# Performance work log

Measured on AMD Instinct MI355X. Metric: run time of the kernel, lower is better.

The kernel has to match this reference:

```python
import jax, jax.numpy as jnp
import numpy as np

V, E, H0, H1 = 32000, 512, 1024, 1024
B, S = 32, 128


def setup_inputs() -> dict:
    key = jax.random.key(0)
    ks = jax.random.split(key, 10)
    s = 0.02
    tokens = jax.random.randint(ks[0], (B, S), 0, V)
    emb = jax.random.normal(ks[1], (V, E), dtype=jnp.float32) * s
    W0 = jax.random.normal(ks[2], (E, H0), dtype=jnp.float32) * s
    U0 = jax.random.normal(ks[3], (H0, H0), dtype=jnp.float32) * s
    b0 = jnp.zeros((H0,), dtype=jnp.float32)
    W1 = jax.random.normal(ks[4], (H0, H1), dtype=jnp.float32) * s
    U1 = jax.random.normal(ks[5], (H1, H1), dtype=jnp.float32) * s
    b1 = jnp.zeros((H1,), dtype=jnp.float32)
    Wd = jax.random.normal(ks[6], (H1, V), dtype=jnp.float32) * s
    bd = jnp.zeros((V,), dtype=jnp.float32)
    return {"tokens": tokens, "emb": emb, "W0": W0, "U0": U0, "b0": b0,
            "W1": W1, "U1": U1, "b1": b1, "Wd": Wd, "bd": bd}


def reference(tokens, emb, W0, U0, b0, W1, U1, b1, Wd, bd):
    # Embedding lookup: [B, S, E]
    x = emb[tokens]
    # Stacked SimpleRNN: h_t = tanh(x W + h U + b), layer1 feeds layer2 per step.
    xt = jnp.swapaxes(x, 0, 1)  # [S, B, E] for scan over time

    def step(carry, x_t):
        h0, h1 = carry
        h0 = jnp.tanh(x_t @ W0 + h0 @ U0 + b0)
        h1 = jnp.tanh(h0 @ W1 + h1 @ U1 + b1)
        return (h0, h1), h1

    batch = tokens.shape[0]
    init = (jnp.zeros((batch, W0.shape[1]), dtype=x.dtype),
            jnp.zeros((batch, W1.shape[1]), dtype=x.dtype))
    _, ys = jax.lax.scan(step, init, xt)  # ys: [S, B, H1]
    ys = jnp.swapaxes(ys, 0, 1)  # [B, S, H1]
    # Final dense to vocab logits: [B, S, V]
    return ys @ Wd + bd
```

## Files before the change

### kernel.cpp

```cpp
#include <hip/hip_runtime.h>
#include <hip/hip_bf16.h>
#include <cstdint>

typedef __attribute__((ext_vector_type(8))) short bf16x8;
typedef __attribute__((ext_vector_type(4))) float f32x4;
typedef __attribute__((ext_vector_type(4))) unsigned int u32x4;

#define V_ 32000
#define E_ 512
#define H_ 1024
#define B_ 32
#define S_ 128

#define L1WG 16
#define L2WG 32
#define NWGS 48
#define NTILES 250
#define GWGS (16 * NTILES)

typedef __attribute__((address_space(1))) unsigned int* gas1_t;
typedef __attribute__((address_space(3))) unsigned int* las3_t;
__device__ __forceinline__ void load_lds16(const void* g, void* l) {
  __builtin_amdgcn_global_load_lds((gas1_t)g, (las3_t)l, 16, 0, 0);
}

__device__ __forceinline__ void ldx4_sc(u32x4* d, const void* p) {
  asm volatile("global_load_dwordx4 %0, %1, off sc0 sc1" : "=v"(*d) : "v"(p) : "memory");
}
__device__ __forceinline__ unsigned ld_sc(const unsigned* p) {
  unsigned d;
  asm volatile("global_load_dword %0, %1, off sc0 sc1\n\ts_waitcnt vmcnt(0)"
               : "=v"(d) : "v"(p) : "memory");
  return d;
}
__device__ __forceinline__ void st_swap(unsigned* p, unsigned v) {
  asm volatile("global_atomic_swap %0, %1, off sc1" :: "v"(p), "v"(v) : "memory");
}
__device__ __forceinline__ void st_swap2(uint2* p, uint2 v) {
  asm volatile("global_atomic_swap_x2 %0, %1, off sc1" :: "v"(p), "v"(v) : "memory");
}
#define WAITVM0()                                     \
  asm volatile("s_waitcnt vmcnt(0)" ::: "memory");    \
  __builtin_amdgcn_sched_barrier(0)

__device__ __forceinline__ unsigned short bfbits(float x) {
  __hip_bfloat16 b = __float2bfloat16(x);
  union { __hip_bfloat16 b; unsigned short u; } c;
  c.b = b;
  return c.u;
}

__device__ __forceinline__ uint2 pack_rows(const float f[4], int lane, int j) {
  uint2 v2[4];
#pragma unroll
  for (int r = 0; r < 4; ++r) {
    const float o = __shfl_xor(f[r], 1);
    const float lo = (lane & 1) ? o : f[r];
    const float hi = (lane & 1) ? f[r] : o;
    const unsigned pk = (unsigned)bfbits(lo) | ((unsigned)bfbits(hi) << 16);
    const unsigned q2 = __shfl_xor(pk, 2);
    v2[r].x = (j & 2) ? q2 : pk;
    v2[r].y = (j & 2) ? pk : q2;
  }
  const int rs = lane & 3;
  return rs == 0 ? v2[0] : rs == 1 ? v2[1] : rs == 2 ? v2[2] : v2[3];
}

__global__ __launch_bounds__(256) void transpose_f32_bf16(
    const float* __restrict__ src, __hip_bfloat16* __restrict__ dst, int R, int C) {
  __shared__ float tile[32][33];
  const int c0 = blockIdx.x << 5, r0 = blockIdx.y << 5;
  const int tx = threadIdx.x & 31, ty = threadIdx.x >> 5;
#pragma unroll
  for (int i = 0; i < 32; i += 8)
    tile[ty + i][tx] = src[(size_t)(r0 + ty + i) * C + (c0 + tx)];
  __syncthreads();
#pragma unroll
  for (int i = 0; i < 32; i += 8)
    dst[(size_t)(c0 + ty + i) * R + (r0 + tx)] = __float2bfloat16(tile[tx][ty + i]);
}

__global__ __launch_bounds__(256) void gather_embed(
    const int* __restrict__ tokens, const float* __restrict__ emb,
    __hip_bfloat16* __restrict__ Xg) {
  const int r = blockIdx.x;
  const int t = r >> 5, b = r & 31;
  const int tok = tokens[b * S_ + t];
  const float* e = emb + (size_t)tok * E_;
  __hip_bfloat16* o = Xg + (size_t)r * E_;
  for (int k = threadIdx.x; k < E_; k += 256) o[k] = __float2bfloat16(e[k]);
}

__global__ __launch_bounds__(256) void make_frag_w(
    const float* __restrict__ W, __hip_bfloat16* __restrict__ F, int ncols) {
  const int idx = blockIdx.x * 256 + threadIdx.x;
  const int lane = idx & 63, kb = (idx >> 6) & 31, g = idx >> 11;
  const int j = (g << 4) + (lane & 15);
  const int kbase = (kb << 5) + ((lane >> 4) << 3);
  __hip_bfloat16* o = F + (size_t)idx * 8;
#pragma unroll
  for (int e = 0; e < 8; ++e) o[e] = __float2bfloat16(W[(size_t)(kbase + e) * ncols + j]);
}

__global__ __launch_bounds__(256) void gemm_bf16_tn(
    const __hip_bfloat16* __restrict__ A, const __hip_bfloat16* __restrict__ Bt,
    const float* __restrict__ bias, float* __restrict__ C, int M, int N, int K) {
  __shared__ __hip_bfloat16 ldsA[2][128 * 64];
  __shared__ __hip_bfloat16 ldsB[2][128 * 64];
  const int nwg = gridDim.x * gridDim.y;
  int L = blockIdx.y * gridDim.x + blockIdx.x;
  L = ((L & 7) * (nwg >> 3)) + (L >> 3);
  const int m0 = (L / gridDim.x) << 7;
  const int n0 = (L % gridDim.x) << 7;
  const int tid = threadIdx.x, wave = tid >> 6, lane = tid & 63;
  const int wr = wave >> 1, wc = wave & 1;
  f32x4 acc[4][4];
#pragma unroll
  for (int i = 0; i < 4; ++i)
#pragma unroll
    for (int jj = 0; jj < 4; ++jj) acc[i][jj] = (f32x4){0.f, 0.f, 0.f, 0.f};

  auto stage = [&](int buf, int k0) {
#pragma unroll
    for (int i = 0; i < 4; ++i) {
      const int c = i * 4 + wave;
      const int idx = (c << 6) + lane;
      const int row = idx >> 3, kk = (idx & 7) << 3;
      load_lds16(A + (size_t)(m0 + row) * K + (k0 + kk), &ldsA[buf][c * 512]);
      load_lds16(Bt + (size_t)(n0 + row) * K + (k0 + kk), &ldsB[buf][c * 512]);
    }
  };
  stage(0, 0);
  __syncthreads();
  int cur = 0;
  for (int k0 = 0; k0 < K; k0 += 64) {
    if (k0 + 64 < K) stage(cur ^ 1, k0 + 64);
    __builtin_amdgcn_s_setprio(1);
#pragma unroll
    for (int ks = 0; ks < 2; ++ks) {
      bf16x8 af[4], bfr[4];
#pragma unroll
      for (int mi = 0; mi < 4; ++mi)
        af[mi] = *(const bf16x8*)(&ldsA[cur][0] +
                                  (((wr << 6) + (mi << 4) + (lane & 15)) << 6) +
                                  (ks << 5) + ((lane >> 4) << 3));
#pragma unroll
      for (int ni = 0; ni < 4; ++ni)
        bfr[ni] = *(const bf16x8*)(&ldsB[cur][0] +
                                   (((wc << 6) + (ni << 4) + (lane & 15)) << 6) +
                                   (ks << 5) + ((lane >> 4) << 3));
#pragma unroll
      for (int mi = 0; mi < 4; ++mi)
#pragma unroll
        for (int ni = 0; ni < 4; ++ni)
          acc[mi][ni] =
              __builtin_amdgcn_mfma_f32_16x16x32_bf16(af[mi], bfr[ni], acc[mi][ni], 0, 0, 0);
    }
    __builtin_amdgcn_s_setprio(0);
    __syncthreads();
    cur ^= 1;
  }
#pragma unroll
  for (int mi = 0; mi < 4; ++mi) {
#pragma unroll
    for (int ni = 0; ni < 4; ++ni) {
      const int n = n0 + (wc << 6) + (ni << 4) + (lane & 15);
      const float bn = bias[n];
#pragma unroll
      for (int r = 0; r < 4; ++r) {
        const int m = m0 + (wr << 6) + (mi << 4) + ((lane >> 4) << 2) + r;
        C[(size_t)m * N + n] = acc[mi][ni][r] + bn;
      }
    }
  }
}

__global__ __launch_bounds__(512, 1) void rnn_vocab_fused(
    const __hip_bfloat16* __restrict__ U0f, const __hip_bfloat16* __restrict__ W1f,
    const __hip_bfloat16* __restrict__ U1f, const float* __restrict__ xw,
    const float* __restrict__ b1,
    __hip_bfloat16* __restrict__ h0buf,
    __hip_bfloat16* __restrict__ h1buf,
    __hip_bfloat16* __restrict__ Yf,
    unsigned* __restrict__ flags,
    const __hip_bfloat16* __restrict__ Wdf,
    const float* __restrict__ bd, float* __restrict__ out) {
  __shared__ char smem[135168];
  const int tid = threadIdx.x, wave = tid >> 6, lane = tid & 63;

  if (blockIdx.x < NWGS) {
    char* sA0 = smem;
    char* sA1 = smem + 65536;
    float* pad = (float*)(smem + 131072);
    const int g = blockIdx.x;
    const bool isL1 = (g < L1WG);
    const int mi = wave & 1;
    const int cg = isL1 ? (wave >> 1) : ((wave >> 1) & 1);
    const int mat = isL1 ? 0 : (wave >> 2);
    const int colbase = isL1 ? (g << 6) : ((g - L1WG) << 5);
    const int j = colbase + (cg << 4) + (lane & 15);
    const int gg = (colbase >> 4) + cg;
    const int rowbase = (mi << 4) + ((lane >> 4) << 2);
    const int rs = lane & 3;
    const int ra = (mi << 4) + (lane & 15);
    const int q4 = (lane >> 4) << 4;
    const float b1j = b1[j];

    const __hip_bfloat16* wb = isL1 ? U0f : (mat == 0 ? W1f : U1f);
    bf16x8 wfr[32];
#pragma unroll
    for (int kb = 0; kb < 32; ++kb)
      wfr[kb] = *(const bf16x8*)(wb + (size_t)((((gg << 5) + kb) << 6) + lane) * 8);

    if (!isL1) {
      for (int i = tid; i < 4096; i += 512) *(uint4*)(sA1 + i * 16) = (uint4){0u, 0u, 0u, 0u};
    }
    __syncthreads();

    const int stg_row = tid >> 7;
    const int stg_colb = (tid & 127) << 4;
    const unsigned* fpoll = flags + ((lane < NWGS ? lane : NWGS - 1) << 4);

    if (isL1) {
      for (int p = 0; p < S_; ++p) {
        const float* xrow = xw + ((size_t)p << 15);
        float xv[4];
#pragma unroll
        for (int r = 0; r < 4; ++r) xv[r] = xrow[(rowbase + r) * H_ + j];
        if (p >= 1) {
          const unsigned tgt =
              (lane < L1WG) ? (unsigned)p : (p >= 3 ? (unsigned)(p - 3) : 0u);
          unsigned v;
          do { v = ld_sc(fpoll); } while (__any(v < tgt));
          const char* src0 = (const char*)(h0buf + ((size_t)((p - 1) & 3) << 15));
          u32x4 t0[8];
#pragma unroll
          for (int i = 0; i < 8; ++i) ldx4_sc(&t0[i], src0 + (size_t)(((i << 9) + tid) << 4));
          WAITVM0();
#pragma unroll
          for (int i = 0; i < 8; ++i) {
            const int row = stg_row + (i << 2);
            *(u32x4*)(sA0 + (row << 11) + (stg_colb ^ ((row & 7) << 4))) = t0[i];
          }
          __syncthreads();
        }
        f32x4 acc = {0.f, 0.f, 0.f, 0.f};
        if (p >= 1) {
#pragma unroll
          for (int kb = 0; kb < 32; ++kb) {
            bf16x8 a = *(const bf16x8*)(
                sA0 + (ra << 11) + ((((kb << 6) + q4)) ^ ((ra & 7) << 4)));
            acc = __builtin_amdgcn_mfma_f32_16x16x32_bf16(a, wfr[kb], acc, 0, 0, 0);
          }
        }
        float f[4];
#pragma unroll
        for (int r = 0; r < 4; ++r) f[r] = tanhf(acc[r] + xv[r]);
        uint2 vsel = pack_rows(f, lane, j);
        uint2* h4 = (uint2*)(h0buf + ((size_t)(p & 3) << 15));
        st_swap2(h4 + (rowbase + rs) * (H_ / 4) + (j >> 2), vsel);
        WAITVM0();
        __syncthreads();
        if (tid == 0) st_swap(flags + (g << 4), (unsigned)(p + 1));
      }
    } else {
      for (int t = 0; t < S_; ++t) {
        {
          const unsigned tgt = (lane < L1WG) ? (unsigned)(t + 1) : (unsigned)t;
          unsigned v;
          do { v = ld_sc(fpoll); } while (__any(v < tgt));
        }
        {
          const char* src0 = (const char*)(h0buf + ((size_t)(t & 3) << 15));
          u32x4 t0[8], t1[8];
#pragma unroll
          for (int i = 0; i < 8; ++i) ldx4_sc(&t0[i], src0 + (size_t)(((i << 9) + tid) << 4));
          if (t >= 1) {
            const char* src1 = (const char*)(h1buf + ((size_t)((t - 1) & 1) << 15));
#pragma unroll
            for (int i = 0; i < 8; ++i) ldx4_sc(&t1[i], src1 + (size_t)(((i << 9) + tid) << 4));
          }
          WAITVM0();
#pragma unroll
          for (int i = 0; i < 8; ++i) {
            const int row = stg_row + (i << 2);
            *(u32x4*)(sA0 + (row << 11) + (stg_colb ^ ((row & 7) << 4))) = t0[i];
          }
          if (t >= 1) {
#pragma unroll
            for (int i = 0; i < 8; ++i) {
              const int row = stg_row + (i << 2);
              *(u32x4*)(sA1 + (row << 11) + (stg_colb ^ ((row & 7) << 4))) = t1[i];
            }
          }
          __syncthreads();
        }
        const char* sA = (mat == 0) ? sA0 : sA1;
        f32x4 acc = {0.f, 0.f, 0.f, 0.f};
#pragma unroll
        for (int kb = 0; kb < 32; ++kb) {
          bf16x8 a = *(const bf16x8*)(
              sA + (ra << 11) + ((((kb << 6) + q4)) ^ ((ra & 7) << 4)));
          acc = __builtin_amdgcn_mfma_f32_16x16x32_bf16(a, wfr[kb], acc, 0, 0, 0);
        }
        const int pair = wave & 3;
        if (mat == 0) *(f32x4*)(pad + pair * 256 + lane * 4) = acc;
        __syncthreads();
        if (mat == 1) {
          f32x4 accW = *(const f32x4*)(pad + pair * 256 + lane * 4);
          float f[4];
#pragma unroll
          for (int r = 0; r < 4; ++r) f[r] = tanhf(acc[r] + accW[r] + b1j);
          uint2 vsel = pack_rows(f, lane, j);
          const int bb = rowbase + rs;
          uint2* h4 = (uint2*)(h1buf + ((size_t)(t & 1) << 15));
          st_swap2(h4 + bb * (H_ / 4) + (j >> 2), vsel);
          const int jb = j & ~3;
          const size_t fo =
              (((size_t)((t << 1) + (bb >> 4)) << 5) + (jb >> 5)) * 64 +
              (((jb >> 3) & 3) << 4) + (bb & 15);
          st_swap2((uint2*)((char*)Yf + fo * 16 + ((jb & 7) << 1)), vsel);
        }
        WAITVM0();
        __syncthreads();
        if (tid == 0) st_swap(flags + (g << 4), (unsigned)(t + 1));
      }
    }
    return;
  }

  const int bid = blockIdx.x - NWGS;
  const int mt = bid / NTILES, nt = bid - mt * NTILES;
  const int m0 = mt << 8, n0 = nt << 7;
  {
    const unsigned tgt = (unsigned)((mt << 3) + 8);
    if (wave == 0) {
      const unsigned* fp = flags + ((L1WG + (lane & 31)) << 4);
      while (true) {
        unsigned v = ld_sc(fp);
        if (!__any(v < tgt)) break;
        asm volatile("s_sleep 8");
      }
    }
    __syncthreads();
  }
  const int wr = wave >> 1, wc = wave & 1;
  f32x4 acc[4][4];
#pragma unroll
  for (int i = 0; i < 4; ++i)
#pragma unroll
    for (int jj = 0; jj < 4; ++jj) acc[i][jj] = (f32x4){0.f, 0.f, 0.f, 0.f};

  const char* Yc = (const char*)Yf;
  const char* Wc = (const char*)Wdf;
  auto stageA = [&](int buf, int k0) {
#pragma unroll
    for (int i = 0; i < 4; ++i) {
      const int c = (i << 3) + wave;
      const int mg = c >> 1, kb = c & 1;
      const char* src = Yc + ((((size_t)(m0 >> 4) + mg) << 5) + (k0 >> 5) + kb) * 1024 +
                        (lane << 4);
      load_lds16(src, smem + buf * 32768 + c * 1024);
    }
  };
  auto stageB = [&](int buf, int k0) {
#pragma unroll
    for (int i = 0; i < 2; ++i) {
      const int c = (i << 3) + wave;
      const int ng = c >> 1, kb = c & 1;
      const char* src = Wc + ((((size_t)(n0 >> 4) + ng) << 5) + (k0 >> 5) + kb) * 1024 +
                        (lane << 4);
      load_lds16(src, smem + 65536 + buf * 16384 + c * 1024);
    }
  };

  stageA(0, 0);
  stageB(0, 0);
  __syncthreads();
  int cur = 0;
  for (int k0 = 0; k0 < H_; k0 += 64) {
    if (k0 + 64 < H_) {
      stageA(cur ^ 1, k0 + 64);
      stageB(cur ^ 1, k0 + 64);
    }
    __builtin_amdgcn_s_setprio(1);
#pragma unroll
    for (int ks = 0; ks < 2; ++ks) {
      bf16x8 af[4], bfr[4];
#pragma unroll
      for (int mi = 0; mi < 4; ++mi)
        af[mi] = *(const bf16x8*)(smem + cur * 32768 +
                                  ((((wr << 2) + mi) << 1) + ks) * 1024 + (lane << 4));
#pragma unroll
      for (int ni = 0; ni < 4; ++ni)
        bfr[ni] = *(const bf16x8*)(smem + 65536 + cur * 16384 +
                                   ((((wc << 2) + ni) << 1) + ks) * 1024 + (lane << 4));
#pragma unroll
      for (int mi = 0; mi < 4; ++mi)
#pragma unroll
        for (int ni = 0; ni < 4; ++ni)
          acc[mi][ni] =
              __builtin_amdgcn_mfma_f32_16x16x32_bf16(af[mi], bfr[ni], acc[mi][ni], 0, 0, 0);
    }
    __builtin_amdgcn_s_setprio(0);
    __syncthreads();
    cur ^= 1;
  }
#pragma unroll
  for (int mi = 0; mi < 4; ++mi) {
#pragma unroll
    for (int ni = 0; ni < 4; ++ni) {
      const int n = n0 + (wc << 6) + (ni << 4) + (lane & 15);
      const float bn = bd[n];
#pragma unroll
      for (int r = 0; r < 4; ++r) {
        const int m = m0 + (wr << 6) + (mi << 4) + ((lane >> 4) << 2) + r;
        const size_t orow = (size_t)(m & 31) * S_ + (m >> 5);
        out[orow * V_ + n] = acc[mi][ni][r] + bn;
      }
    }
  }
}

extern "C" void kernel_launch(void* const* d_in, const int* in_sizes, int n_in, void* d_out,
                              int out_size, void* d_ws, size_t ws_size, hipStream_t stream) {
  const int* tokens = (const int*)d_in[0];
  const float* emb = (const float*)d_in[1];
  const float* W0 = (const float*)d_in[2];
  const float* U0 = (const float*)d_in[3];
  const float* b0 = (const float*)d_in[4];
  const float* W1 = (const float*)d_in[5];
  const float* U1 = (const float*)d_in[6];
  const float* b1 = (const float*)d_in[7];
  const float* Wd = (const float*)d_in[8];
  const float* bd = (const float*)d_in[9];
  float* out = (float*)d_out;

  char* ws = (char*)d_ws;
  __hip_bfloat16* Wdf = (__hip_bfloat16*)ws;  ws += (size_t)V_ * H_ * 2;
  __hip_bfloat16* W0t = (__hip_bfloat16*)ws;  ws += (size_t)H_ * E_ * 2;
  __hip_bfloat16* Xg = (__hip_bfloat16*)ws;   ws += (size_t)4096 * E_ * 2;
  __hip_bfloat16* U0f = (__hip_bfloat16*)ws;  ws += (size_t)H_ * H_ * 2;
  __hip_bfloat16* W1f = (__hip_bfloat16*)ws;  ws += (size_t)H_ * H_ * 2;
  __hip_bfloat16* U1f = (__hip_bfloat16*)ws;  ws += (size_t)H_ * H_ * 2;
  float* xw = (float*)ws;                     ws += (size_t)4096 * H_ * 4;
  __hip_bfloat16* h0buf = (__hip_bfloat16*)ws; ws += 4 * B_ * H_ * 2;
  __hip_bfloat16* h1buf = (__hip_bfloat16*)ws; ws += 2 * B_ * H_ * 2;
  __hip_bfloat16* Yf = (__hip_bfloat16*)ws;   ws += (size_t)4096 * H_ * 2;
  unsigned* flags = (unsigned*)ws;            ws += 4096;

  transpose_f32_bf16<<<dim3(H_ / 32, E_ / 32), 256, 0, stream>>>(W0, W0t, E_, H_);
  gather_embed<<<4096, 256, 0, stream>>>(tokens, emb, Xg);
  make_frag_w<<<512, 256, 0, stream>>>(U0, U0f, H_);
  make_frag_w<<<512, 256, 0, stream>>>(W1, W1f, H_);
  make_frag_w<<<512, 256, 0, stream>>>(U1, U1f, H_);
  make_frag_w<<<16000, 256, 0, stream>>>(Wd, Wdf, V_);
  hipMemsetAsync(flags, 0, 4096, stream);

  gemm_bf16_tn<<<dim3(H_ / 128, 4096 / 128), 256, 0, stream>>>(Xg, W0t, b0, xw, 4096, H_, E_);

  rnn_vocab_fused<<<NWGS + GWGS, 512, 0, stream>>>(U0f, W1f, U1f, xw, b1, h0buf, h1buf, Yf,
                                                   flags, Wdf, bd, out);
}
```

Before: 1.084 ms.

## Make output GEMM persistent over N-tiles with deeper prefetch pipeline

Replaces the 4000 one-tile GEMM workgroups with 208 persistent workgroups. Each one loops over its N-tiles and all 16 M-tiles in order, waiting on the RNN progress flags before each M-tile. The K loop now prefetches two stages ahead, using explicit vmcnt(6) waits and split barriers in place of a full wait each iteration. This is meant to cut launch and scheduling overhead, keep the Wd tile hot across M-tiles, and overlap loads with MFMA. The risk is load imbalance, since 250 tiles over 208 workgroups leaves some with two tiles, and the ordering is stricter against RNN completion.

```diff
diff --git a/kernel.cpp b/kernel.cpp
--- a/kernel.cpp
+++ b/kernel.cpp
@@ -16,7 +16,7 @@
 #define L2WG 32
 #define NWGS 48
 #define NTILES 250
-#define GWGS (16 * NTILES)
+#define GWGS 208
 
 typedef __attribute__((address_space(1))) unsigned int* gas1_t;
 typedef __attribute__((address_space(3))) unsigned int* las3_t;
@@ -41,6 +41,9 @@
 }
 #define WAITVM0()                                     \
   asm volatile("s_waitcnt vmcnt(0)" ::: "memory");    \
+  __builtin_amdgcn_sched_barrier(0)
+#define WAITVM6()                                     \
+  asm volatile("s_waitcnt vmcnt(6)" ::: "memory");    \
   __builtin_amdgcn_sched_barrier(0)
 
 __device__ __forceinline__ unsigned short bfbits(float x) {
@@ -329,94 +332,111 @@
     return;
   }
 
-  const int bid = blockIdx.x - NWGS;
-  const int mt = bid / NTILES, nt = bid - mt * NTILES;
-  const int m0 = mt << 8, n0 = nt << 7;
-  {
-    const unsigned tgt = (unsigned)((mt << 3) + 8);
-    if (wave == 0) {
-      const unsigned* fp = flags + ((L1WG + (lane & 31)) << 4);
-      while (true) {
-        unsigned v = ld_sc(fp);
-        if (!__any(v < tgt)) break;
-        asm volatile("s_sleep 8");
-      }
-    }
-    __syncthreads();
-  }
+  const int wg = blockIdx.x - NWGS;
   const int wr = wave >> 1, wc = wave & 1;
-  f32x4 acc[4][4];
-#pragma unroll
-  for (int i = 0; i < 4; ++i)
-#pragma unroll
-    for (int jj = 0; jj < 4; ++jj) acc[i][jj] = (f32x4){0.f, 0.f, 0.f, 0.f};
-
   const char* Yc = (const char*)Yf;
   const char* Wc = (const char*)Wdf;
-  auto stageA = [&](int buf, int k0) {
-#pragma unroll
-    for (int i = 0; i < 4; ++i) {
-      const int c = (i << 3) + wave;
-      const int mg = c >> 1, kb = c & 1;
-      const char* src = Yc + ((((size_t)(m0 >> 4) + mg) << 5) + (k0 >> 5) + kb) * 1024 +
-                        (lane << 4);
-      load_lds16(src, smem + buf * 32768 + c * 1024);
-    }
-  };
-  auto stageB = [&](int buf, int k0) {
-#pragma unroll
-    for (int i = 0; i < 2; ++i) {
-      const int c = (i << 3) + wave;
-      const int ng = c >> 1, kb = c & 1;
-      const char* src = Wc + ((((size_t)(n0 >> 4) + ng) << 5) + (k0 >> 5) + kb) * 1024 +
-                        (lane << 4);
-      load_lds16(src, smem + 65536 + buf * 16384 + c * 1024);
-    }
-  };
-
-  stageA(0, 0);
-  stageB(0, 0);
-  __syncthreads();
-  int cur = 0;
-  for (int k0 = 0; k0 < H_; k0 += 64) {
-    if (k0 + 64 < H_) {
-      stageA(cur ^ 1, k0 + 64);
-      stageB(cur ^ 1, k0 + 64);
-    }
-    __builtin_amdgcn_s_setprio(1);
-#pragma unroll
-    for (int ks = 0; ks < 2; ++ks) {
-      bf16x8 af[4], bfr[4];
-#pragma unroll
-      for (int mi = 0; mi < 4; ++mi)
-        af[mi] = *(const bf16x8*)(smem + cur * 32768 +
-                                  ((((wr << 2) + mi) << 1) + ks) * 1024 + (lane << 4));
-#pragma unroll
-      for (int ni = 0; ni < 4; ++ni)
-        bfr[ni] = *(const bf16x8*)(smem + 65536 + cur * 16384 +
-                                   ((((wc << 2) + ni) << 1) + ks) * 1024 + (lane << 4));
-#pragma unroll
-      for (int mi = 0; mi < 4; ++mi)
-#pragma unroll
-        for (int ni = 0; ni < 4; ++ni)
-          acc[mi][ni] =
-              __builtin_amdgcn_mfma_f32_16x16x32_bf16(af[mi], bfr[ni], acc[mi][ni], 0, 0, 0);
-    }
-    __builtin_amdgcn_s_setprio(0);
-    __syncthreads();
-    cur ^= 1;
-  }
-#pragma unroll
-  for (int mi = 0; mi < 4; ++mi) {
-#pragma unroll
-    for (int ni = 0; ni < 4; ++ni) {
-      const int n = n0 + (wc << 6) + (ni << 4) + (lane & 15);
-      const float bn = bd[n];
-#pragma unroll
-      for (int r = 0; r < 4; ++r) {
-        const int m = m0 + (wr << 6) + (mi << 4) + ((lane >> 4) << 2) + r;
-        const size_t orow = (size_t)(m & 31) * S_ + (m >> 5);
-        out[orow * V_ + n] = acc[mi][ni][r] + bn;
+
+  for (int nt = wg; nt < NTILES; nt += GWGS) {
+    const int n0 = nt << 7;
+    for (int mt = 0; mt < 16; ++mt) {
+      const int m0 = mt << 8;
+      {
+        const unsigned tgt = (unsigned)((mt << 3) + 8);
+        if (wave == 0) {
+          const unsigned* fp = flags + ((L1WG + (lane & 31)) << 4);
+          while (true) {
+            unsigned v = ld_sc(fp);
+            if (!__any(v < tgt)) break;
+            asm volatile("s_sleep 4");
+          }
+        }
+        __syncthreads();
+      }
+      f32x4 acc[4][4];
+#pragma unroll
+      for (int i = 0; i < 4; ++i)
+#pragma unroll
+        for (int jj = 0; jj < 4; ++jj) acc[i][jj] = (f32x4){0.f, 0.f, 0.f, 0.f};
+
+      auto stageA = [&](int buf, int k0) {
+#pragma unroll
+        for (int i = 0; i < 4; ++i) {
+          const int c = (i << 3) + wave;
+          const char* src = Yc +
+              ((((size_t)(m0 >> 4) + (c >> 1)) << 5) + (k0 >> 5) + (c & 1)) * 1024 +
+              (lane << 4);
+          load_lds16(src, smem + buf * 32768 + c * 1024);
+        }
+      };
+      auto stageB = [&](int buf, int k0) {
+#pragma unroll
+        for (int i = 0; i < 2; ++i) {
+          const int c = (i << 3) + wave;
+          const char* src = Wc +
+              ((((size_t)(n0 >> 4) + (c >> 1)) << 5) + (k0 >> 5) + (c & 1)) * 1024 +
+              (lane << 4);
+          load_lds16(src, smem + 65536 + buf * 16384 + c * 1024);
+        }
+      };
+
+      stageA(0, 0);
+      stageB(0, 0);
+      stageA(1, 64);
+      stageB(1, 64);
+      WAITVM6();
+      __builtin_amdgcn_sched_barrier(0);
+      __builtin_amdgcn_s_barrier();
+      int cur = 0;
+      for (int k0 = 0; k0 < H_; k0 += 64) {
+        __builtin_amdgcn_s_setprio(1);
+#pragma unroll
+        for (int ks = 0; ks < 2; ++ks) {
+          bf16x8 af[4], bfr[4];
+#pragma unroll
+          for (int mi = 0; mi < 4; ++mi)
+            af[mi] = *(const bf16x8*)(smem + cur * 32768 +
+                                      ((((wr << 2) + mi) << 1) + ks) * 1024 + (lane << 4));
+#pragma unroll
+          for (int ni = 0; ni < 4; ++ni)
+            bfr[ni] = *(const bf16x8*)(smem + 65536 + cur * 16384 +
+                                       ((((wc << 2) + ni) << 1) + ks) * 1024 + (lane << 4));
+#pragma unroll
+          for (int mi = 0; mi < 4; ++mi)
+#pragma unroll
+            for (int ni = 0; ni < 4; ++ni)
+              acc[mi][ni] = __builtin_amdgcn_mfma_f32_16x16x32_bf16(af[mi], bfr[ni],
+                                                                    acc[mi][ni], 0, 0, 0);
+        }
+        __builtin_amdgcn_s_setprio(0);
+        if (k0 + 64 < H_) {
+          __builtin_amdgcn_sched_barrier(0);
+          __builtin_amdgcn_s_barrier();
+          if (k0 + 128 < H_) {
+            stageA(cur, k0 + 128);
+            stageB(cur, k0 + 128);
+            WAITVM6();
+          } else {
+            WAITVM0();
+          }
+          __builtin_amdgcn_sched_barrier(0);
+          __builtin_amdgcn_s_barrier();
+          cur ^= 1;
+        }
+      }
+#pragma unroll
+      for (int mi = 0; mi < 4; ++mi) {
+#pragma unroll
+        for (int ni = 0; ni < 4; ++ni) {
+          const int n = n0 + (wc << 6) + (ni << 4) + (lane & 15);
+          const float bn = bd[n];
+#pragma unroll
+          for (int r = 0; r < 4; ++r) {
+            const int m = m0 + (wr << 6) + (mi << 4) + ((lane >> 4) << 2) + r;
+            const size_t orow = (size_t)(m & 31) * S_ + (m >> 5);
+            out[orow * V_ + n] = acc[mi][ni][r] + bn;
+          }
+        }
       }
     }
   }
```

Result: slower. 1.393 ms (+28.5%).
